# Kernel tuning notes

Hardware: AMD Instinct MI355X
Metric: run time of the kernel (lower is better)

Reference implementation:

```python
import jax, jax.numpy as jnp
import numpy as np

D_MODEL = 1024
NUM_HEAD = 16
HEAD_DIM = D_MODEL // NUM_HEAD  # 64


def setup_inputs() -> dict:
    key = jax.random.key(0)
    ks = jax.random.split(key, 9)
    B, S = 2, 2048
    s = 0.02
    return {
        "x": jax.random.normal(ks[0], (B, S, D_MODEL), dtype=jnp.float32),
        "Wq": jax.random.normal(ks[1], (D_MODEL, D_MODEL), dtype=jnp.float32) * s,
        "bq": jax.random.normal(ks[2], (D_MODEL,), dtype=jnp.float32) * s,
        "Wk": jax.random.normal(ks[3], (D_MODEL, D_MODEL), dtype=jnp.float32) * s,
        "bk": jax.random.normal(ks[4], (D_MODEL,), dtype=jnp.float32) * s,
        "Wv": jax.random.normal(ks[5], (D_MODEL, D_MODEL), dtype=jnp.float32) * s,
        "bv": jax.random.normal(ks[6], (D_MODEL,), dtype=jnp.float32) * s,
        "Wo": jax.random.normal(ks[7], (D_MODEL, D_MODEL), dtype=jnp.float32) * s,
        "bo": jax.random.normal(ks[8], (D_MODEL,), dtype=jnp.float32) * s,
    }


def _split_head(t):
    # [B,S,D] -> [B,H,S,hd]
    B, S, _ = t.shape
    return t.reshape(B, S, NUM_HEAD, HEAD_DIM).transpose(0, 2, 1, 3)


def reference(x, Wq, bq, Wk, bk, Wv, bv, Wo, bo):
    B, S, D = x.shape
    q = _split_head(x @ Wq.T + bq)  # [B,H,S,hd]
    k = _split_head(x @ Wk.T + bk)
    v = _split_head(x @ Wv.T + bv)
    scale = 1.0 / jnp.sqrt(jnp.asarray(HEAD_DIM, dtype=x.dtype))
    scores = jnp.einsum("bhqd,bhkd->bhqk", q, k) * scale  # [B,H,S,S]
    attn = jax.nn.softmax(scores, axis=-1)
    out = jnp.einsum("bhqk,bhkd->bhqd", attn, v)  # [B,H,S,hd]
    out = out.transpose(0, 2, 1, 3).reshape(B, S, D)
    return out @ Wo.T + bo
```

## Files before the change

### kernel.cpp

```cpp
#include <hip/hip_runtime.h>
#include <cstdint>


typedef unsigned short ush;
typedef __bf16 bf16x8 __attribute__((ext_vector_type(8)));
typedef float f32x4 __attribute__((ext_vector_type(4)));
typedef ush u16x8 __attribute__((ext_vector_type(8)));
typedef ush u16x4 __attribute__((ext_vector_type(4)));

__device__ __forceinline__ ush f2bf(float f) {
  unsigned int u = __float_as_uint(f);
  u += 0x7fffu + ((u >> 16) & 1u);
  return (ush)(u >> 16);
}

__device__ __forceinline__ unsigned int pack2bf(float a, float b) {
  return (unsigned int)f2bf(a) | ((unsigned int)f2bf(b) << 16);
}

__device__ __forceinline__ bf16x8 bc8(u16x8 v) {
  return __builtin_bit_cast(bf16x8, v);
}

__device__ __forceinline__ void async16(const void* g, void* l) {
  __builtin_amdgcn_global_load_lds(
      (const __attribute__((address_space(1))) unsigned int*)(uintptr_t)g,
      (__attribute__((address_space(3))) unsigned int*)(uintptr_t)l, 16, 0, 0);
}

__global__ __launch_bounds__(256) void convert_kernel(
    const float* __restrict__ x, const float* __restrict__ Wq,
    const float* __restrict__ Wk, const float* __restrict__ Wv,
    const float* __restrict__ Wo,
    ush* __restrict__ xb, ush* __restrict__ Wqb, ush* __restrict__ Wkb,
    ush* __restrict__ Wvb, ush* __restrict__ Wob)
{
  int tid = blockIdx.x * 256 + threadIdx.x;
  int base = tid * 4;
  const float* src; ush* dst; int idx;
  if (base < 4194304) { src = x; dst = xb; idx = base; }
  else {
    int r = base - 4194304;
    int seg = r >> 20;
    idx = r & 1048575;
    src = seg == 0 ? Wq : seg == 1 ? Wk : seg == 2 ? Wv : Wo;
    dst = seg == 0 ? Wqb : seg == 1 ? Wkb : seg == 2 ? Wvb : Wob;
  }
  float4 f = *(const float4*)(src + idx);
  u16x4 u = { f2bf(f.x), f2bf(f.y), f2bf(f.z), f2bf(f.w) };
  *(u16x4*)(dst + idx) = u;
}

__device__ __forceinline__ void gemm128_core(
    const ush* __restrict__ gA, const ush* __restrict__ gB,
    int m0, int n0, ush* lA, ush* lB, f32x4 (&acc)[4][4])
{
  const int t = threadIdx.x, w = t >> 6, lane = t & 63;
  const int l15 = lane & 15, quad = lane >> 4;
  const int wm = (w >> 1) * 64, wn = (w & 1) * 64;
#pragma unroll
  for (int i = 0; i < 4; ++i)
#pragma unroll
    for (int j = 0; j < 4; ++j) acc[i][j] = (f32x4){0.f, 0.f, 0.f, 0.f};

  for (int kt = 0; kt < 1024; kt += 64) {
#pragma unroll
    for (int i = 0; i < 4; ++i) {
      int j = i * 256 + w * 64 + lane;
      int row = j >> 3, cc = (j & 7) ^ (row & 7);
      async16(gA + (size_t)(m0 + row) * 1024 + kt + cc * 8,
              lA + (i * 256 + w * 64) * 8);
    }
#pragma unroll
    for (int i = 0; i < 4; ++i) {
      int j = i * 256 + w * 64 + lane;
      int row = j >> 3, cc = (j & 7) ^ (row & 7);
      async16(gB + (size_t)(n0 + row) * 1024 + kt + cc * 8,
              lB + (i * 256 + w * 64) * 8);
    }
    __syncthreads();
#pragma unroll
    for (int kf = 0; kf < 2; ++kf) {
      bf16x8 aF[4], bF[4];
#pragma unroll
      for (int mt = 0; mt < 4; ++mt) {
        int row = wm + mt * 16 + l15;
        aF[mt] = bc8(*(const u16x8*)(lA + row * 64 + (((kf * 4 + quad) ^ (row & 7)) * 8)));
      }
#pragma unroll
      for (int nt = 0; nt < 4; ++nt) {
        int row = wn + nt * 16 + l15;
        bF[nt] = bc8(*(const u16x8*)(lB + row * 64 + (((kf * 4 + quad) ^ (row & 7)) * 8)));
      }
#pragma unroll
      for (int mt = 0; mt < 4; ++mt)
#pragma unroll
        for (int nt = 0; nt < 4; ++nt)
          acc[mt][nt] = __builtin_amdgcn_mfma_f32_16x16x32_bf16(
              aF[mt], bF[nt], acc[mt][nt], 0, 0, 0);
    }
    __syncthreads();
  }
}

__global__ __launch_bounds__(256, 2) void qkv_gemm(
    const ush* __restrict__ xb, const ush* __restrict__ Wqb,
    const ush* __restrict__ Wkb, const ush* __restrict__ Wvb,
    const float* __restrict__ bq, const float* __restrict__ bk,
    const float* __restrict__ bv,
    ush* __restrict__ q, ush* __restrict__ k, ush* __restrict__ vt)
{
  int bid = blockIdx.x;
  int wsel = bid >> 8;
  int rem = bid & 255;
  int m0 = (rem & 31) * 128;
  int n0 = (rem >> 5) * 128;
  const ush* gB = wsel == 0 ? Wqb : wsel == 1 ? Wkb : Wvb;
  const float* bias = wsel == 0 ? bq : wsel == 1 ? bk : bv;
  const float oscale = wsel == 1 ? 0.180336880f : 1.0f;

  __shared__ alignas(16) ush lA[128 * 64];
  __shared__ alignas(16) ush lB[128 * 64];
  f32x4 acc[4][4];
  gemm128_core(xb, gB, m0, n0, lA, lB, acc);

  const int t = threadIdx.x, w = t >> 6, lane = t & 63;
  const int l15 = lane & 15, quad = lane >> 4;
  const int wm = (w >> 1) * 64, wn = (w & 1) * 64;
  if (wsel == 2) {
#pragma unroll
    for (int nt = 0; nt < 4; ++nt) {
      int o = n0 + wn + nt * 16 + l15;
      float bl = bias[o];
      int h = o >> 6, d = o & 63;
#pragma unroll
      for (int mt = 0; mt < 4; ++mt) {
        int tb = m0 + wm + mt * 16 + quad * 4;
        int b = tb >> 11, s = tb & 2047;
        u16x4 pk = { f2bf(acc[mt][nt][0] + bl), f2bf(acc[mt][nt][1] + bl),
                     f2bf(acc[mt][nt][2] + bl), f2bf(acc[mt][nt][3] + bl) };
        *(u16x4*)(vt + (size_t)(((b * 16 + h) * 64) + d) * 2048 + s) = pk;
      }
    }
  } else {
    ush* dst = wsel == 0 ? q : k;
#pragma unroll
    for (int nt = 0; nt < 4; ++nt) {
      int o = n0 + wn + nt * 16 + l15;
      float bl = bias[o];
      int h = o >> 6, d = o & 63;
#pragma unroll
      for (int mt = 0; mt < 4; ++mt)
#pragma unroll
        for (int r = 0; r < 4; ++r) {
          int token = m0 + wm + mt * 16 + quad * 4 + r;
          int b = token >> 11, s = token & 2047;
          dst[(size_t)(((b * 16 + h) * 2048) + s) * 64 + d] =
              f2bf((acc[mt][nt][r] + bl) * oscale);
        }
    }
  }
}

__global__ __launch_bounds__(256, 4) void attn_kernel(
    const ush* __restrict__ Q, const ush* __restrict__ K,
    const ush* __restrict__ VT, ush* __restrict__ O)
{
  const int bid = blockIdx.x;
  const int bh = (bid & 7) * 4 + (bid >> 8);
  const int qt = (bid >> 3) & 31;
  const ush* qb = Q + (size_t)bh * 2048 * 64;
  const ush* kb = K + (size_t)bh * 2048 * 64;
  const ush* vtb = VT + (size_t)bh * 64 * 2048;
  const int t = threadIdx.x, w = t >> 6, lane = t & 63;
  const int l15 = lane & 15, quad = lane >> 4;
  const int q0 = qt * 64 + w * 16;

  __shared__ alignas(16) ush lK[64 * 64];
  __shared__ alignas(16) ush lV[64 * 64];
  __shared__ alignas(16) ush lP[4][16 * 64];

  const int r0 = t >> 3;
  const int c0 = (t & 7) ^ (r0 & 7);

  bf16x8 qF[2];
#pragma unroll
  for (int kf = 0; kf < 2; ++kf)
    qF[kf] = bc8(*(const u16x8*)(qb + (size_t)(q0 + l15) * 64 + kf * 32 + quad * 8));

  float li = 0.f;
  f32x4 accO[4];
#pragma unroll
  for (int dt = 0; dt < 4; ++dt) accO[dt] = (f32x4){0.f, 0.f, 0.f, 0.f};

  u16x8 kr0 = *(const u16x8*)(kb + (size_t)r0 * 64 + c0 * 8);
  u16x8 kr1 = *(const u16x8*)(kb + (size_t)(r0 + 32) * 64 + c0 * 8);
  u16x8 vr0 = *(const u16x8*)(vtb + (size_t)r0 * 2048 + c0 * 8);
  u16x8 vr1 = *(const u16x8*)(vtb + (size_t)(r0 + 32) * 2048 + c0 * 8);
  *(u16x8*)(lK + t * 8) = kr0;
  *(u16x8*)(lK + (t + 256) * 8) = kr1;
  *(u16x8*)(lV + t * 8) = vr0;
  *(u16x8*)(lV + (t + 256) * 8) = vr1;
  __syncthreads();

  for (int kt = 0; kt < 2048; kt += 64) {
    const int ktn = kt + 64;
    if (ktn < 2048) {
      kr0 = *(const u16x8*)(kb + (size_t)(ktn + r0) * 64 + c0 * 8);
      kr1 = *(const u16x8*)(kb + (size_t)(ktn + r0 + 32) * 64 + c0 * 8);
      vr0 = *(const u16x8*)(vtb + (size_t)r0 * 2048 + ktn + c0 * 8);
      vr1 = *(const u16x8*)(vtb + (size_t)(r0 + 32) * 2048 + ktn + c0 * 8);
    }

    f32x4 sc[4];
#pragma unroll
    for (int mt = 0; mt < 4; ++mt) sc[mt] = (f32x4){0.f, 0.f, 0.f, 0.f};
#pragma unroll
    for (int kf = 0; kf < 2; ++kf) {
#pragma unroll
      for (int mt = 0; mt < 4; ++mt) {
        int row = mt * 16 + l15;
        bf16x8 aK = bc8(*(const u16x8*)(lK + row * 64 + (((kf * 4 + quad) ^ (row & 7)) * 8)));
        sc[mt] = __builtin_amdgcn_mfma_f32_16x16x32_bf16(aK, qF[kf], sc[mt], 0, 0, 0);
      }
    }

    float rs = 0.f;
#pragma unroll
    for (int mt = 0; mt < 4; ++mt) {
      f32x4 p;
#pragma unroll
      for (int r = 0; r < 4; ++r) { p[r] = exp2f(sc[mt][r]); rs += p[r]; }
      uint2 pw = { pack2bf(p[0], p[1]), pack2bf(p[2], p[3]) };
      int chunk = mt * 2 + (quad >> 1);
      *(uint2*)(&lP[w][l15 * 64 + ((chunk ^ (l15 & 7)) * 8) + (quad & 1) * 4]) = pw;
    }
    rs += __shfl_xor(rs, 16);
    rs += __shfl_xor(rs, 32);
    li += rs;

    __builtin_amdgcn_wave_barrier();

    bf16x8 aP[2];
#pragma unroll
    for (int kf = 0; kf < 2; ++kf)
      aP[kf] = bc8(*(const u16x8*)(&lP[w][l15 * 64 + (((kf * 4 + quad) ^ (l15 & 7)) * 8)]));
#pragma unroll
    for (int kf = 0; kf < 2; ++kf) {
#pragma unroll
      for (int dt = 0; dt < 4; ++dt) {
        int row = dt * 16 + l15;
        bf16x8 bV = bc8(*(const u16x8*)(lV + row * 64 + (((kf * 4 + quad) ^ (row & 7)) * 8)));
        accO[dt] = __builtin_amdgcn_mfma_f32_16x16x32_bf16(aP[kf], bV, accO[dt], 0, 0, 0);
      }
    }
    __syncthreads();
    if (ktn < 2048) {
      *(u16x8*)(lK + t * 8) = kr0;
      *(u16x8*)(lK + (t + 256) * 8) = kr1;
      *(u16x8*)(lV + t * 8) = vr0;
      *(u16x8*)(lV + (t + 256) * 8) = vr1;
    }
    __syncthreads();
  }

  const int b = bh >> 4, h = bh & 15;
  float linv[4];
#pragma unroll
  for (int r = 0; r < 4; ++r)
    linv[r] = __builtin_amdgcn_rcpf(__shfl(li, quad * 4 + r));
#pragma unroll
  for (int dt = 0; dt < 4; ++dt)
#pragma unroll
    for (int r = 0; r < 4; ++r) {
      int s = q0 + quad * 4 + r;
      O[(size_t)(b * 2048 + s) * 1024 + h * 64 + dt * 16 + l15] =
          f2bf(accO[dt][r] * linv[r]);
    }
}

__global__ __launch_bounds__(256, 2) void out_gemm(
    const ush* __restrict__ ab, const ush* __restrict__ Wob,
    const float* __restrict__ bo, float* __restrict__ out)
{
  int rem = blockIdx.x;
  int m0 = (rem & 31) * 128;
  int n0 = (rem >> 5) * 128;
  __shared__ alignas(16) ush lA[128 * 64];
  __shared__ alignas(16) ush lB[128 * 64];
  f32x4 acc[4][4];
  gemm128_core(ab, Wob, m0, n0, lA, lB, acc);

  const int t = threadIdx.x, w = t >> 6, lane = t & 63;
  const int l15 = lane & 15, quad = lane >> 4;
  const int wm = (w >> 1) * 64, wn = (w & 1) * 64;
#pragma unroll
  for (int nt = 0; nt < 4; ++nt) {
    int o = n0 + wn + nt * 16 + l15;
    float bl = bo[o];
#pragma unroll
    for (int mt = 0; mt < 4; ++mt)
#pragma unroll
      for (int r = 0; r < 4; ++r) {
        int token = m0 + wm + mt * 16 + quad * 4 + r;
        out[(size_t)token * 1024 + o] = acc[mt][nt][r] + bl;
      }
  }
}

extern "C" void kernel_launch(void* const* d_in, const int* in_sizes, int n_in,
                              void* d_out, int out_size, void* d_ws, size_t ws_size,
                              hipStream_t stream)
{
  const float* x  = (const float*)d_in[0];
  const float* Wq = (const float*)d_in[1];
  const float* bq = (const float*)d_in[2];
  const float* Wk = (const float*)d_in[3];
  const float* bk = (const float*)d_in[4];
  const float* Wv = (const float*)d_in[5];
  const float* bv = (const float*)d_in[6];
  const float* Wo = (const float*)d_in[7];
  const float* bo = (const float*)d_in[8];
  float* out = (float*)d_out;

  char* ws = (char*)d_ws;
  ush* xb  = (ush*)(ws);
  ush* Wqb = (ush*)(ws + (size_t)( 8u << 20));
  ush* Wkb = (ush*)(ws + (size_t)(10u << 20));
  ush* Wvb = (ush*)(ws + (size_t)(12u << 20));
  ush* Wob = (ush*)(ws + (size_t)(14u << 20));
  ush* qb  = (ush*)(ws + (size_t)(16u << 20));
  ush* kb  = (ush*)(ws + (size_t)(24u << 20));
  ush* vtb = (ush*)(ws + (size_t)(32u << 20));
  ush* ab  = (ush*)(ws + (size_t)(40u << 20));

  convert_kernel<<<8192, 256, 0, stream>>>(x, Wq, Wk, Wv, Wo,
                                           xb, Wqb, Wkb, Wvb, Wob);
  qkv_gemm<<<768, 256, 0, stream>>>(xb, Wqb, Wkb, Wvb, bq, bk, bv, qb, kb, vtb);
  attn_kernel<<<1024, 256, 0, stream>>>(qb, kb, vtb, ab);
  out_gemm<<<256, 256, 0, stream>>>(ab, Wob, bo, out);
}
```

Measured before the change: 207.4 us.

## Double-buffer K/V tiles with async global-to-LDS loads in attention

Replaces the register-staged K/V prefetch in the attention kernel with direct global_load_lds transfers into a double-buffered LDS tile. This drops one of the two barriers per iteration and frees the VGPRs that held the staged tile. It also swaps exp2f for the raw hardware exp2 builtin and uses a cheaper round-half-up bf16 pack built on v_perm. LDS use doubles for K/V, which may limit occupancy. The code relies on the barrier at the end of each iteration to make the async loads visible, with no explicit vmcnt wait.

Result: faster. 188.2 us (-9.3%).

```diff
diff --git a/kernel.cpp b/kernel.cpp
--- a/kernel.cpp
+++ b/kernel.cpp
@@ -14,8 +14,10 @@
   return (ush)(u >> 16);
 }
 
-__device__ __forceinline__ unsigned int pack2bf(float a, float b) {
-  return (unsigned int)f2bf(a) | ((unsigned int)f2bf(b) << 16);
+__device__ __forceinline__ unsigned int pack2bf_ru(float a, float b) {
+  unsigned int ua = __float_as_uint(a) + 0x8000u;
+  unsigned int ub = __float_as_uint(b) + 0x8000u;
+  return __builtin_amdgcn_perm(ub, ua, 0x07060302u);
 }
 
 __device__ __forceinline__ bf16x8 bc8(u16x8 v) {
@@ -176,12 +178,16 @@
   const int l15 = lane & 15, quad = lane >> 4;
   const int q0 = qt * 64 + w * 16;
 
-  __shared__ alignas(16) ush lK[64 * 64];
-  __shared__ alignas(16) ush lV[64 * 64];
+  __shared__ alignas(16) ush lK[2][64 * 64];
+  __shared__ alignas(16) ush lV[2][64 * 64];
   __shared__ alignas(16) ush lP[4][16 * 64];
 
   const int r0 = t >> 3;
   const int c0 = (t & 7) ^ (r0 & 7);
+  const ush* kSrc0 = kb + (size_t)r0 * 64 + c0 * 8;
+  const ush* kSrc1 = kb + (size_t)(r0 + 32) * 64 + c0 * 8;
+  const ush* vSrc0 = vtb + (size_t)r0 * 2048 + c0 * 8;
+  const ush* vSrc1 = vtb + (size_t)(r0 + 32) * 2048 + c0 * 8;
 
   bf16x8 qF[2];
 #pragma unroll
@@ -193,24 +199,24 @@
 #pragma unroll
   for (int dt = 0; dt < 4; ++dt) accO[dt] = (f32x4){0.f, 0.f, 0.f, 0.f};
 
-  u16x8 kr0 = *(const u16x8*)(kb + (size_t)r0 * 64 + c0 * 8);
-  u16x8 kr1 = *(const u16x8*)(kb + (size_t)(r0 + 32) * 64 + c0 * 8);
-  u16x8 vr0 = *(const u16x8*)(vtb + (size_t)r0 * 2048 + c0 * 8);
-  u16x8 vr1 = *(const u16x8*)(vtb + (size_t)(r0 + 32) * 2048 + c0 * 8);
-  *(u16x8*)(lK + t * 8) = kr0;
-  *(u16x8*)(lK + (t + 256) * 8) = kr1;
-  *(u16x8*)(lV + t * 8) = vr0;
-  *(u16x8*)(lV + (t + 256) * 8) = vr1;
+  async16(kSrc0, lK[0] + t * 8);
+  async16(kSrc1, lK[0] + (t + 256) * 8);
+  async16(vSrc0, lV[0] + t * 8);
+  async16(vSrc1, lV[0] + (t + 256) * 8);
   __syncthreads();
 
-  for (int kt = 0; kt < 2048; kt += 64) {
-    const int ktn = kt + 64;
-    if (ktn < 2048) {
-      kr0 = *(const u16x8*)(kb + (size_t)(ktn + r0) * 64 + c0 * 8);
-      kr1 = *(const u16x8*)(kb + (size_t)(ktn + r0 + 32) * 64 + c0 * 8);
-      vr0 = *(const u16x8*)(vtb + (size_t)r0 * 2048 + ktn + c0 * 8);
-      vr1 = *(const u16x8*)(vtb + (size_t)(r0 + 32) * 2048 + ktn + c0 * 8);
-    }
+  for (int it = 0; it < 32; ++it) {
+    const int cur = it & 1, nxt = cur ^ 1;
+    if (it + 1 < 32) {
+      const size_t ko = (size_t)(it + 1) * 64 * 64;
+      const int vo = (it + 1) * 64;
+      async16(kSrc0 + ko, lK[nxt] + t * 8);
+      async16(kSrc1 + ko, lK[nxt] + (t + 256) * 8);
+      async16(vSrc0 + vo, lV[nxt] + t * 8);
+      async16(vSrc1 + vo, lV[nxt] + (t + 256) * 8);
+    }
+    const ush* lk = lK[cur];
+    const ush* lv = lV[cur];
 
     f32x4 sc[4];
 #pragma unroll
@@ -220,7 +226,7 @@
 #pragma unroll
       for (int mt = 0; mt < 4; ++mt) {
         int row = mt * 16 + l15;
-        bf16x8 aK = bc8(*(const u16x8*)(lK + row * 64 + (((kf * 4 + quad) ^ (row & 7)) * 8)));
+        bf16x8 aK = bc8(*(const u16x8*)(lk + row * 64 + (((kf * 4 + quad) ^ (row & 7)) * 8)));
         sc[mt] = __builtin_amdgcn_mfma_f32_16x16x32_bf16(aK, qF[kf], sc[mt], 0, 0, 0);
       }
     }
@@ -230,8 +236,11 @@
     for (int mt = 0; mt < 4; ++mt) {
       f32x4 p;
 #pragma unroll
-      for (int r = 0; r < 4; ++r) { p[r] = exp2f(sc[mt][r]); rs += p[r]; }
-      uint2 pw = { pack2bf(p[0], p[1]), pack2bf(p[2], p[3]) };
+      for (int r = 0; r < 4; ++r) {
+        p[r] = __builtin_amdgcn_exp2f(sc[mt][r]);
+        rs += p[r];
+      }
+      uint2 pw = { pack2bf_ru(p[0], p[1]), pack2bf_ru(p[2], p[3]) };
       int chunk = mt * 2 + (quad >> 1);
       *(uint2*)(&lP[w][l15 * 64 + ((chunk ^ (l15 & 7)) * 8) + (quad & 1) * 4]) = pw;
     }
@@ -250,16 +259,9 @@
 #pragma unroll
       for (int dt = 0; dt < 4; ++dt) {
         int row = dt * 16 + l15;
-        bf16x8 bV = bc8(*(const u16x8*)(lV + row * 64 + (((kf * 4 + quad) ^ (row & 7)) * 8)));
+        bf16x8 bV = bc8(*(const u16x8*)(lv + row * 64 + (((kf * 4 + quad) ^ (row & 7)) * 8)));
         accO[dt] = __builtin_amdgcn_mfma_f32_16x16x32_bf16(aP[kf], bV, accO[dt], 0, 0, 0);
       }
-    }
-    __syncthreads();
-    if (ktn < 2048) {
-      *(u16x8*)(lK + t * 8) = kr0;
-      *(u16x8*)(lK + (t + 256) * 8) = kr1;
-      *(u16x8*)(lV + t * 8) = vr0;
-      *(u16x8*)(lV + (t + 256) * 8) = vr1;
     }
     __syncthreads();
   }
```
